# Kernel optimization log

Measured on AMD Instinct MI355X. Metric: run time of the kernel, lower is better.

Reference implementation:

```python
import jax, jax.numpy as jnp
import numpy as np
import math

D_MODEL = 1024
N_HEADS = 16
D_HEAD = D_MODEL // N_HEADS
LSR_RANK = 32
B, T = 4, 2048


def setup_inputs() -> dict:
    key = jax.random.key(0)
    ks = jax.random.split(key, 11)
    s = 1.0 / math.sqrt(D_MODEL)
    x = jax.random.normal(ks[0], (B, T, D_MODEL), dtype=jnp.float32)
    Wq = jax.random.uniform(ks[1], (D_MODEL, D_MODEL), minval=-s, maxval=s)
    bq = jax.random.uniform(ks[2], (D_MODEL,), minval=-s, maxval=s)
    Wk = jax.random.uniform(ks[3], (D_MODEL, D_MODEL), minval=-s, maxval=s)
    bk = jax.random.uniform(ks[4], (D_MODEL,), minval=-s, maxval=s)
    Wv = jax.random.uniform(ks[5], (D_MODEL, D_MODEL), minval=-s, maxval=s)
    bv = jax.random.uniform(ks[6], (D_MODEL,), minval=-s, maxval=s)
    Wo = jax.random.uniform(ks[7], (D_MODEL, D_MODEL), minval=-s, maxval=s)
    bo = jax.random.uniform(ks[8], (D_MODEL,), minval=-s, maxval=s)
    Wq_lsr = jax.random.normal(ks[9], (N_HEADS, D_HEAD, LSR_RANK)) / math.sqrt(D_HEAD)
    Wk_lsr = jax.random.normal(ks[10], (N_HEADS, D_HEAD, LSR_RANK)) / math.sqrt(D_HEAD)
    return {"x": x, "Wq": Wq, "bq": bq, "Wk": Wk, "bk": bk,
            "Wv": Wv, "bv": bv, "Wo": Wo, "bo": bo,
            "Wq_lsr": Wq_lsr, "Wk_lsr": Wk_lsr}


def reference(x, Wq, bq, Wk, bk, Wv, bv, Wo, bo, Wq_lsr, Wk_lsr):
    Bq, Tq, _ = x.shape
    # Linear projections (torch Linear: x @ W.T + b), split into heads -> (B,H,T,Dh)
    def split_heads(y):
        return y.reshape(Bq, Tq, N_HEADS, D_HEAD).transpose(0, 2, 1, 3)
    q = split_heads(x @ Wq.T + bq)
    k = split_heads(x @ Wk.T + bk)
    v = split_heads(x @ Wv.T + bv)
    # LSR: project q,k to rank-R per head
    q_lr = jnp.einsum('bhtd,hdr->bhtr', q, Wq_lsr)
    k_lr = jnp.einsum('bhtd,hdr->bhtr', k, Wk_lsr)
    scale = 1.0 / math.sqrt(max(LSR_RANK, 1))
    scores = jnp.einsum('bhir,bhjr->bhij', q_lr, k_lr) * scale  # (B,H,T,T)
    causal_mask = jnp.triu(jnp.ones((Tq, Tq), dtype=bool), k=1)
    scores = jnp.where(causal_mask, jnp.float32(-jnp.inf), scores)
    attn = jax.nn.softmax(scores, axis=-1)
    y = jnp.einsum('bhij,bhjd->bhid', attn, v)  # (B,H,T,Dh)
    y = y.transpose(0, 2, 1, 3).reshape(Bq, Tq, D_MODEL)
    return y @ Wo.T + bo
```

## Files before the change

### kernel.cpp

```cpp
#include <hip/hip_runtime.h>

#define B_  4
#define T_  2048
#define H_  16
#define DM_ 1024
#define DH_ 64
#define RK_ 32

using u16 = unsigned short;
using u32 = unsigned int;
typedef float  floatx4 __attribute__((ext_vector_type(4)));
typedef __bf16 bf16x8  __attribute__((ext_vector_type(8)));
typedef u16    u16x8   __attribute__((ext_vector_type(8)));
typedef u16    u16x4   __attribute__((ext_vector_type(4)));
typedef short  s16x4   __attribute__((ext_vector_type(4)));

#define MFMA16(a,b,c) __builtin_amdgcn_mfma_f32_16x16x32_bf16((a),(b),(c),0,0,0)
#define MFMA1K(a,b,c) __builtin_amdgcn_mfma_f32_16x16x16bf16_1k((a),(b),(c),0,0,0)

__device__ __forceinline__ u16 f2bf(float f) {
  unsigned u = __float_as_uint(f);
  u += 0x7fffu + ((u >> 16) & 1u);
  return (u16)(u >> 16);
}
__device__ __forceinline__ float b2f(u16 h) {
  return __uint_as_float(((unsigned)h) << 16);
}
__device__ __forceinline__ u32 pack_bf(float a, float b) {
  u32 ua = __float_as_uint(a); ua += 0x7fffu + ((ua >> 16) & 1u);
  u32 ub = __float_as_uint(b); ub += 0x7fffu + ((ub >> 16) & 1u);
  return __builtin_amdgcn_perm(ub, ua, 0x07060302u);
}
__device__ __forceinline__ u32 tpack(float a, float b) {
  return __builtin_amdgcn_perm(__float_as_uint(b), __float_as_uint(a), 0x07060302u);
}

__device__ __forceinline__ void async_copy16(const u16* g, const u16* lds_uniform_base) {
  __builtin_amdgcn_global_load_lds(
      (const __attribute__((address_space(1))) unsigned int*)(unsigned long long)g,
      (__attribute__((address_space(3))) unsigned int*)(unsigned int)(unsigned long long)lds_uniform_base,
      16, 0, 0);
}

__global__ __launch_bounds__(256) void cvt_x(const float* __restrict__ s,
                                             u16* __restrict__ d, int n4) {
  int i = blockIdx.x * 256 + threadIdx.x;
  if (i >= n4) return;
  float4 v = reinterpret_cast<const float4*>(s)[i];
  u16x4 o = { f2bf(v.x), f2bf(v.y), f2bf(v.z), f2bf(v.w) };
  reinterpret_cast<u16x4*>(d)[i] = o;
}

__global__ __launch_bounds__(256) void cvt_weights(const float* __restrict__ Wq,
                                                   const float* __restrict__ Wk,
                                                   const float* __restrict__ Wv,
                                                   const float* __restrict__ Wo,
                                                   u16* __restrict__ Wcat) {
  int i = blockIdx.x * 256 + threadIdx.x;
  int reg = i >> 18;
  const float* s = (reg == 0) ? Wq : (reg == 1) ? Wk : (reg == 2) ? Wv : Wo;
  int j = i & 262143;
  float4 v = reinterpret_cast<const float4*>(s)[j];
  u16x4 o = { f2bf(v.x), f2bf(v.y), f2bf(v.z), f2bf(v.w) };
  reinterpret_cast<u16x4*>(Wcat)[i] = o;
}

template <int OUTF32>
__global__ __launch_bounds__(256, 2) void gemm_bt(const u16* __restrict__ A,
                                                  const u16* __restrict__ W,
                                                  const float* __restrict__ b0,
                                                  const float* __restrict__ b1,
                                                  const float* __restrict__ b2,
                                                  void* __restrict__ Cv, int ldc) {
  __shared__ __align__(16) u16 Al[128 * 32];
  __shared__ __align__(16) u16 Bl[128 * 32];
  const int tid  = threadIdx.x;
  const int lane = tid & 63;
  const int wave = tid >> 6;
  const int quad = lane >> 4;
  const int l16  = lane & 15;
  const int wm   = (wave >> 1) << 6;
  const int wn   = (wave & 1) << 6;
  const int bm   = blockIdx.x * 128;
  const int bn   = blockIdx.y * 128;

  floatx4 acc[4][4];
#pragma unroll
  for (int i = 0; i < 4; i++)
#pragma unroll
    for (int j = 0; j < 4; j++) acc[i][j] = (floatx4){0.f, 0.f, 0.f, 0.f};

  const u16* Ag[2]; const u16* Wg[2]; u16* Alb[2]; u16* Blb[2];
#pragma unroll
  for (int issue = 0; issue < 2; issue++) {
    int c = issue * 256 + tid;
    Ag[issue]  = A + (size_t)(bm + (c >> 2)) * 1024 + (c & 3) * 8;
    Wg[issue]  = W + (size_t)(bn + (c >> 2)) * 1024 + (c & 3) * 8;
    int ub = (issue * 256 + wave * 64) * 8;
    Alb[issue] = Al + ub;
    Blb[issue] = Bl + ub;
  }

  for (int k0 = 0; k0 < 1024; k0 += 32) {
#pragma unroll
    for (int issue = 0; issue < 2; issue++) {
      async_copy16(Ag[issue] + k0, Alb[issue]);
      async_copy16(Wg[issue] + k0, Blb[issue]);
    }
    __syncthreads();
    bf16x8 af[4], bfr[4];
#pragma unroll
    for (int i = 0; i < 4; i++) {
      af[i]  = *reinterpret_cast<const bf16x8*>(Al + (wm + i * 16 + l16) * 32 + quad * 8);
      bfr[i] = *reinterpret_cast<const bf16x8*>(Bl + (wn + i * 16 + l16) * 32 + quad * 8);
    }
#pragma unroll
    for (int mi = 0; mi < 4; mi++)
#pragma unroll
      for (int ni = 0; ni < 4; ni++)
        acc[mi][ni] = MFMA16(af[mi], bfr[ni], acc[mi][ni]);
    __syncthreads();
  }

  const float* bp = (bn < 1024) ? b0 : ((bn < 2048) ? b1 : b2);
#pragma unroll
  for (int ni = 0; ni < 4; ni++) {
    int col = bn + wn + ni * 16 + l16;
    float bias = bp[col & 1023];
#pragma unroll
    for (int mi = 0; mi < 4; mi++)
#pragma unroll
      for (int r = 0; r < 4; r++) {
        int row = bm + wm + mi * 16 + quad * 4 + r;
        float v = acc[mi][ni][r] + bias;
        if (OUTF32)
          reinterpret_cast<float*>(Cv)[(size_t)row * ldc + col] = v;
        else
          reinterpret_cast<u16*>(Cv)[(size_t)row * ldc + col] = f2bf(v);
      }
  }
}

__global__ __launch_bounds__(256) void vtrans(const u16* __restrict__ qkv,
                                              u16* __restrict__ vt) {
  const int tb = blockIdx.x;
  const int bh = blockIdx.y;
  const int b = bh >> 4, h = bh & 15;
  __shared__ u16 Vl[64][72];
  const int tid = threadIdx.x;
#pragma unroll
  for (int it = 0; it < 2; it++) {
    int c = it * 256 + tid;
    int t = c >> 3, dc = (c & 7) * 8;
    u16x8 v = *reinterpret_cast<const u16x8*>(
        qkv + (size_t)(b * T_ + tb * 64 + t) * 3072 + 2048 + h * 64 + dc);
    *reinterpret_cast<u16x8*>(&Vl[t][dc]) = v;
  }
  __syncthreads();
#pragma unroll
  for (int it = 0; it < 2; it++) {
    int c = it * 256 + tid;
    int d = c >> 3, tt = (c & 7) * 8;
    u16x8 o;
#pragma unroll
    for (int j = 0; j < 8; j++) o[j] = Vl[tt + j][d];
    *reinterpret_cast<u16x8*>(vt + ((size_t)bh * 64 + d) * T_ + tb * 64 + tt) = o;
  }
}

__global__ __launch_bounds__(256) void lsr_mfma(const u16* __restrict__ qkv,
                                                const float* __restrict__ Wql,
                                                const float* __restrict__ Wkl,
                                                u16* __restrict__ qlr,
                                                u16* __restrict__ klr) {
  const int t0 = blockIdx.x * 128;
  const int bh = blockIdx.y, b = bh >> 4, h = bh & 15;
  const int sel = blockIdx.z;
  const int tid = threadIdx.x, lane = tid & 63, w = tid >> 6;
  const int quad = lane >> 4, l16 = lane & 15;
  __shared__ __align__(16) u16 Al[128 * 64];
  __shared__ __align__(16) u16 Wl[32 * 72];

  const float* Wsrc = (sel ? Wkl : Wql) + h * 2048;
  const float fold = sel ? 1.0f : 0.25506100790944405f;
  {
    float4 a = *reinterpret_cast<const float4*>(Wsrc + tid * 8);
    float4 c = *reinterpret_cast<const float4*>(Wsrc + tid * 8 + 4);
    float vals[8] = {a.x, a.y, a.z, a.w, c.x, c.y, c.z, c.w};
#pragma unroll
    for (int i = 0; i < 8; i++) {
      int idx = tid * 8 + i, d = idx >> 5, r = idx & 31;
      Wl[r * 72 + d] = f2bf(vals[i] * fold);
    }
  }
#pragma unroll
  for (int issue = 0; issue < 4; issue++) {
    int l = issue * 256 + tid;
    int t = l >> 3, ck = l & 7;
    const u16* src = qkv + (size_t)(b * T_ + t0 + t) * 3072 + sel * 1024 + h * 64 +
                     ((ck ^ (t & 7)) * 8);
    async_copy16(src, Al + issue * 2048 + w * 512);
  }
  __syncthreads();

  bf16x8 wf[2][2], af[2][2];
#pragma unroll
  for (int mr = 0; mr < 2; mr++)
#pragma unroll
    for (int c = 0; c < 2; c++)
      wf[mr][c] = *reinterpret_cast<const bf16x8*>(&Wl[(mr * 16 + l16) * 72 + c * 32 + quad * 8]);
#pragma unroll
  for (int i = 0; i < 2; i++) {
    int t = (2 * w + i) * 16 + l16;
#pragma unroll
    for (int c = 0; c < 2; c++)
      af[i][c] = *reinterpret_cast<const bf16x8*>(&Al[t * 64 + (((4 * c + quad) ^ (t & 7)) * 8)]);
  }
  floatx4 acc[2][2];
#pragma unroll
  for (int i = 0; i < 2; i++)
#pragma unroll
    for (int mr = 0; mr < 2; mr++) acc[i][mr] = (floatx4){0.f, 0.f, 0.f, 0.f};
#pragma unroll
  for (int i = 0; i < 2; i++)
#pragma unroll
    for (int mr = 0; mr < 2; mr++)
#pragma unroll
      for (int c = 0; c < 2; c++)
        acc[i][mr] = MFMA16(wf[mr][c], af[i][c], acc[i][mr]);

  u16* outp = sel ? klr : qlr;
#pragma unroll
  for (int i = 0; i < 2; i++) {
    int t = t0 + (2 * w + i) * 16 + l16;
#pragma unroll
    for (int mr = 0; mr < 2; mr++) {
      uint2 pv = { pack_bf(acc[i][mr][0], acc[i][mr][1]),
                   pack_bf(acc[i][mr][2], acc[i][mr][3]) };
      *reinterpret_cast<uint2*>(outp + ((size_t)bh * T_ + t) * 32 + mr * 16 + quad * 4) = pv;
    }
  }
}

__global__ __launch_bounds__(256, 4) void attn(const u16* __restrict__ qlr,
                                               const u16* __restrict__ klr,
                                               const u16* __restrict__ vt,
                                               u16* __restrict__ yatt) {
  const int bh = blockIdx.y;
  const int b = bh >> 4, h = bh & 15;
  const int p = blockIdx.x;
  const int tid = threadIdx.x, lane = tid & 63, w = tid >> 6;
  const int quad = lane >> 4, l16 = lane & 15;

  __shared__ __align__(16) u16 Vt3[3][4096];
  __shared__ __align__(16) u16 Kt3[3][2048];

  const u16* qlr_bh = qlr + (size_t)bh * T_ * RK_;
  const u16* klr_bh = klr + (size_t)bh * T_ * RK_;
  const u16* vt_bh  = vt + (size_t)bh * 64 * T_;

  int voff[4][4];
#pragma unroll
  for (int nt = 0; nt < 4; nt++)
#pragma unroll
    for (int dt = 0; dt < 4; dt++) {
      int d = dt * 16 + l16;
      voff[nt][dt] = d * 64 + (((nt * 2 + (quad >> 1)) ^ (d & 7)) * 8) + (quad & 1) * 4;
    }
  int soffV[2];
#pragma unroll
  for (int issue = 0; issue < 2; issue++) {
    int L = issue * 256 + tid;
    int d = L >> 3, cg = L & 7;
    soffV[issue] = d * T_ + ((cg ^ (d & 7)) * 8);
  }
  const int soffK = (w * 8 + (lane >> 3)) * 64 + (((lane & 7) ^ (lane >> 3)) * 8);
  const int koff = (l16 >> 1) * 64 + ((((l16 & 1) * 4 + quad) ^ (l16 >> 1)) * 8);
  const int wub = w * 512;

  const floatx4 fzero = {0.f, 0.f, 0.f, 0.f};

  for (int run = 0; run < 2; run++) {
    const int qi = run ? p : 31 - p;
    const int q0 = qi * 64;
    if (run) __syncthreads();

    bf16x8 qf = *reinterpret_cast<const bf16x8*>(
        qlr_bh + (size_t)(q0 + w * 16 + l16) * 32 + quad * 8);

    auto stage = [&](int t, int bi) {
      const u16* vs = vt_bh + t * 64;
      async_copy16(vs + soffV[0], &Vt3[bi][wub]);
      async_copy16(vs + soffV[1], &Vt3[bi][2048 + wub]);
      async_copy16(klr_bh + t * 2048 + soffK, &Kt3[bi][wub]);
    };

    stage(0, 0);
    if (qi >= 1) {
      stage(1, 1);
      asm volatile("s_waitcnt vmcnt(3)" ::: "memory");
    } else {
      asm volatile("s_waitcnt vmcnt(0)" ::: "memory");
    }
    __builtin_amdgcn_s_barrier();
    asm volatile("" ::: "memory");

    floatx4 oacc[4];
#pragma unroll
    for (int i = 0; i < 4; i++) oacc[i] = fzero;
    float rs = 0.f;

    const u16* Vb = &Vt3[0][0];
    const u16* Kb = &Kt3[0][0];
    int cb = 0, sb = 2;

    for (int i = 0; i < qi; i++) {
      const bool do_stage = (i + 2 <= qi);
      if (do_stage) stage(i + 2, sb);

      bf16x8 kf[4];
#pragma unroll
      for (int nt = 0; nt < 4; nt++)
        kf[nt] = *reinterpret_cast<const bf16x8*>(Kb + koff + nt * 512);
      floatx4 sv[4];
#pragma unroll
      for (int nt = 0; nt < 4; nt++) sv[nt] = MFMA16(kf[nt], qf, fzero);

      uint2 pk[4];
#pragma unroll
      for (int nt = 0; nt < 4; nt++) {
        float p0 = __builtin_amdgcn_exp2f(sv[nt][0]);
        float p1 = __builtin_amdgcn_exp2f(sv[nt][1]);
        float p2 = __builtin_amdgcn_exp2f(sv[nt][2]);
        float p3 = __builtin_amdgcn_exp2f(sv[nt][3]);
        rs += (p0 + p1) + (p2 + p3);
        pk[nt].x = tpack(p0, p1);
        pk[nt].y = tpack(p2, p3);
      }
#pragma unroll
      for (int dt = 0; dt < 4; dt++)
#pragma unroll
        for (int nt = 0; nt < 4; nt++) {
          s16x4 vf = *reinterpret_cast<const s16x4*>(Vb + voff[nt][dt]);
          oacc[dt] = MFMA1K(vf, __builtin_bit_cast(s16x4, pk[nt]), oacc[dt]);
        }

      if (do_stage) asm volatile("s_waitcnt vmcnt(3)" ::: "memory");
      else          asm volatile("s_waitcnt vmcnt(0)" ::: "memory");
      __builtin_amdgcn_s_barrier();
      asm volatile("" ::: "memory");

      cb = (cb == 2) ? 0 : cb + 1;
      Vb = &Vt3[cb][0];
      Kb = &Kt3[cb][0];
      if (do_stage) sb = (sb == 2) ? 0 : sb + 1;
    }

    {
      bf16x8 kf[4];
#pragma unroll
      for (int nt = 0; nt < 4; nt++)
        kf[nt] = *reinterpret_cast<const bf16x8*>(Kb + koff + nt * 512);
      floatx4 sv[4];
#pragma unroll
      for (int nt = 0; nt < 4; nt++) sv[nt] = MFMA16(kf[nt], qf, fzero);
      const int thr = w * 16 + l16;
      uint2 pk[4];
#pragma unroll
      for (int nt = 0; nt < 4; nt++) {
        float pr[4];
#pragma unroll
        for (int r = 0; r < 4; r++) {
          float e = __builtin_amdgcn_exp2f(sv[nt][r]);
          pr[r] = (nt * 16 + quad * 4 + r <= thr) ? e : 0.f;
        }
        rs += (pr[0] + pr[1]) + (pr[2] + pr[3]);
        pk[nt].x = tpack(pr[0], pr[1]);
        pk[nt].y = tpack(pr[2], pr[3]);
      }
#pragma unroll
      for (int dt = 0; dt < 4; dt++)
#pragma unroll
        for (int nt = 0; nt < 4; nt++) {
          s16x4 vf = *reinterpret_cast<const s16x4*>(Vb + voff[nt][dt]);
          oacc[dt] = MFMA1K(vf, __builtin_bit_cast(s16x4, pk[nt]), oacc[dt]);
        }
    }

    rs += __shfl_xor(rs, 16);
    rs += __shfl_xor(rs, 32);
    float inv = 1.f / rs;
    const int qrow = q0 + w * 16 + l16;
#pragma unroll
    for (int dt = 0; dt < 4; dt++) {
      uint2 ov = { pack_bf(oacc[dt][0] * inv, oacc[dt][1] * inv),
                   pack_bf(oacc[dt][2] * inv, oacc[dt][3] * inv) };
      *reinterpret_cast<uint2*>(
          yatt + (size_t)(b * T_ + qrow) * 1024 + h * 64 + dt * 16 + quad * 4) = ov;
    }
  }
}

extern "C" void kernel_launch(void* const* d_in, const int* in_sizes, int n_in,
                              void* d_out, int out_size, void* d_ws, size_t ws_size,
                              hipStream_t stream) {
  const float* x   = (const float*)d_in[0];
  const float* Wq  = (const float*)d_in[1];
  const float* bq  = (const float*)d_in[2];
  const float* Wk  = (const float*)d_in[3];
  const float* bk  = (const float*)d_in[4];
  const float* Wv  = (const float*)d_in[5];
  const float* bv  = (const float*)d_in[6];
  const float* Wo  = (const float*)d_in[7];
  const float* bo  = (const float*)d_in[8];
  const float* Wql = (const float*)d_in[9];
  const float* Wkl = (const float*)d_in[10];
  float* out = (float*)d_out;

  char* ws = (char*)d_ws;
  u16* xb   = (u16*)(ws);
  u16* Wcat = (u16*)(ws + 16777216);
  u16* qkv  = (u16*)(ws + 25165824);
  u16* qlr  = (u16*)(ws + 75497472);
  u16* klr  = (u16*)(ws + 83886080);
  u16* yatt = (u16*)(ws + 92274688);
  u16* vt   = xb;

  cvt_x<<<dim3(8192), 256, 0, stream>>>(x, xb, 2097152);
  cvt_weights<<<dim3(4096), 256, 0, stream>>>(Wq, Wk, Wv, Wo, Wcat);
  gemm_bt<0><<<dim3(64, 24), 256, 0, stream>>>(xb, Wcat, bq, bk, bv, qkv, 3072);
  vtrans<<<dim3(32, 64), 256, 0, stream>>>(qkv, vt);
  lsr_mfma<<<dim3(16, 64, 2), 256, 0, stream>>>(qkv, Wql, Wkl, qlr, klr);
  attn<<<dim3(16, 64), 256, 0, stream>>>(qlr, klr, vt, yatt);
  gemm_bt<1><<<dim3(64, 8), 256, 0, stream>>>(yatt, Wcat + 3145728, bo, bo, bo, out, 1024);
}
```

Baseline: 272.6 us.

## Double-buffer GEMM with swizzled LDS, K=64 tiles, XCD-aware block remap

Rewrites the bf16 projection GEMM to stage K=64 slices into double-buffered shared memory. The next slice is prefetched while MFMAs run on the current one, and each loop iteration now ends with one barrier instead of two. The LDS layout uses an XOR swizzle to avoid bank conflicts. A 1D grid is remapped so consecutive blocks on the same XCD share tiles, and s_setprio is raised around the MFMA bursts. The catch is that LDS per block grows to 64KB, which may limit occupancy to 2 blocks per CU.

```diff
diff --git a/kernel.cpp b/kernel.cpp
--- a/kernel.cpp
+++ b/kernel.cpp
@@ -66,23 +66,48 @@
 }
 
 template <int OUTF32>
-__global__ __launch_bounds__(256, 2) void gemm_bt(const u16* __restrict__ A,
-                                                  const u16* __restrict__ W,
-                                                  const float* __restrict__ b0,
-                                                  const float* __restrict__ b1,
-                                                  const float* __restrict__ b2,
-                                                  void* __restrict__ Cv, int ldc) {
-  __shared__ __align__(16) u16 Al[128 * 32];
-  __shared__ __align__(16) u16 Bl[128 * 32];
+__global__ __launch_bounds__(256, 2) void gemm8(const u16* __restrict__ A,
+                                                const u16* __restrict__ W,
+                                                const float* __restrict__ b0,
+                                                const float* __restrict__ b1,
+                                                const float* __restrict__ b2,
+                                                void* __restrict__ Cv, int ldc) {
+  __shared__ __align__(16) u16 Al[2][8192];
+  __shared__ __align__(16) u16 Bl[2][8192];
   const int tid  = threadIdx.x;
   const int lane = tid & 63;
-  const int wave = tid >> 6;
+  const int w    = tid >> 6;
   const int quad = lane >> 4;
   const int l16  = lane & 15;
-  const int wm   = (wave >> 1) << 6;
-  const int wn   = (wave & 1) << 6;
-  const int bm   = blockIdx.x * 128;
-  const int bn   = blockIdx.y * 128;
+  const int wm   = (w >> 1) << 6;
+  const int wn   = (w & 1) << 6;
+
+  const int cpx = gridDim.x >> 3;
+  const int idx = (blockIdx.x & 7) * cpx + (blockIdx.x >> 3);
+  const int bm  = (idx & 63) << 7;
+  const int bn  = (idx >> 6) << 7;
+
+  const int sr = tid >> 3;
+  const int sc = ((tid & 7) ^ (sr & 7)) * 8;
+  const u16* Ag = A + (size_t)(bm + sr) * 1024 + sc;
+  const u16* Wg = W + (size_t)(bn + sr) * 1024 + sc;
+
+  auto stage = [&](int k0, int bsel) {
+#pragma unroll
+    for (int j = 0; j < 4; j++)
+      async_copy16(Ag + (size_t)j * 32768 + k0, &Al[bsel][j * 2048 + w * 512]);
+#pragma unroll
+    for (int j = 0; j < 4; j++)
+      async_copy16(Wg + (size_t)j * 32768 + k0, &Bl[bsel][j * 2048 + w * 512]);
+  };
+
+  int aoff[4], boff[4], sl[2];
+#pragma unroll
+  for (int mi = 0; mi < 4; mi++) aoff[mi] = (wm + mi * 16 + l16) * 64;
+#pragma unroll
+  for (int ni = 0; ni < 4; ni++) boff[ni] = (wn + ni * 16 + l16) * 64;
+  sl[0] = ((0 + quad) ^ (l16 & 7)) * 8;
+  sl[1] = ((4 + quad) ^ (l16 & 7)) * 8;
 
   floatx4 acc[4][4];
 #pragma unroll
@@ -90,36 +115,37 @@
 #pragma unroll
     for (int j = 0; j < 4; j++) acc[i][j] = (floatx4){0.f, 0.f, 0.f, 0.f};
 
-  const u16* Ag[2]; const u16* Wg[2]; u16* Alb[2]; u16* Blb[2];
-#pragma unroll
-  for (int issue = 0; issue < 2; issue++) {
-    int c = issue * 256 + tid;
-    Ag[issue]  = A + (size_t)(bm + (c >> 2)) * 1024 + (c & 3) * 8;
-    Wg[issue]  = W + (size_t)(bn + (c >> 2)) * 1024 + (c & 3) * 8;
-    int ub = (issue * 256 + wave * 64) * 8;
-    Alb[issue] = Al + ub;
-    Blb[issue] = Bl + ub;
-  }
-
-  for (int k0 = 0; k0 < 1024; k0 += 32) {
-#pragma unroll
-    for (int issue = 0; issue < 2; issue++) {
-      async_copy16(Ag[issue] + k0, Alb[issue]);
-      async_copy16(Wg[issue] + k0, Blb[issue]);
-    }
-    __syncthreads();
-    bf16x8 af[4], bfr[4];
-#pragma unroll
-    for (int i = 0; i < 4; i++) {
-      af[i]  = *reinterpret_cast<const bf16x8*>(Al + (wm + i * 16 + l16) * 32 + quad * 8);
-      bfr[i] = *reinterpret_cast<const bf16x8*>(Bl + (wn + i * 16 + l16) * 32 + quad * 8);
-    }
-#pragma unroll
-    for (int mi = 0; mi < 4; mi++)
+  stage(0, 0);
+  asm volatile("s_waitcnt vmcnt(0)" ::: "memory");
+  __builtin_amdgcn_s_barrier();
+  asm volatile("" ::: "memory");
+
+  for (int i = 0; i < 16; i++) {
+    if (i < 15) stage((i + 1) * 64, (i + 1) & 1);
+    const u16* Ab = Al[i & 1];
+    const u16* Bb = Bl[i & 1];
+#pragma unroll
+    for (int ks = 0; ks < 2; ks++) {
+      bf16x8 af[4], bfr[4];
+#pragma unroll
+      for (int mi = 0; mi < 4; mi++)
+        af[mi] = *reinterpret_cast<const bf16x8*>(Ab + aoff[mi] + sl[ks]);
 #pragma unroll
       for (int ni = 0; ni < 4; ni++)
-        acc[mi][ni] = MFMA16(af[mi], bfr[ni], acc[mi][ni]);
-    __syncthreads();
+        bfr[ni] = *reinterpret_cast<const bf16x8*>(Bb + boff[ni] + sl[ks]);
+      __builtin_amdgcn_s_setprio(1);
+#pragma unroll
+      for (int mi = 0; mi < 4; mi++)
+#pragma unroll
+        for (int ni = 0; ni < 4; ni++)
+          acc[mi][ni] = MFMA16(af[mi], bfr[ni], acc[mi][ni]);
+      __builtin_amdgcn_s_setprio(0);
+    }
+    if (i < 15) {
+      asm volatile("s_waitcnt vmcnt(0)" ::: "memory");
+      __builtin_amdgcn_s_barrier();
+      asm volatile("" ::: "memory");
+    }
   }
 
   const float* bp = (bn < 1024) ? b0 : ((bn < 2048) ? b1 : b2);
@@ -428,9 +454,9 @@
 
   cvt_x<<<dim3(8192), 256, 0, stream>>>(x, xb, 2097152);
   cvt_weights<<<dim3(4096), 256, 0, stream>>>(Wq, Wk, Wv, Wo, Wcat);
-  gemm_bt<0><<<dim3(64, 24), 256, 0, stream>>>(xb, Wcat, bq, bk, bv, qkv, 3072);
+  gemm8<0><<<dim3(1536), 256, 0, stream>>>(xb, Wcat, bq, bk, bv, qkv, 3072);
   vtrans<<<dim3(32, 64), 256, 0, stream>>>(qkv, vt);
   lsr_mfma<<<dim3(16, 64, 2), 256, 0, stream>>>(qkv, Wql, Wkl, qlr, klr);
   attn<<<dim3(16, 64), 256, 0, stream>>>(qlr, klr, vt, yatt);
-  gemm_bt<1><<<dim3(64, 8), 256, 0, stream>>>(yatt, Wcat + 3145728, bo, bo, bo, out, 1024);
-}
+  gemm8<1><<<dim3(512), 256, 0, stream>>>(yatt, Wcat + 3145728, bo, bo, bo, out, 1024);
+}
```

Result: no change. 270.8 us (-0.7%).
